# Kernel optimization log

Hardware: AMD Instinct MI355X
Metric: run time of the kernel (lower is better)

Reference implementation:

```python
import jax, jax.numpy as jnp
import numpy as np

L = 50
RHO = 1.0

def _get_index():
    # S = {(m,n) | |mn| <= rho*L//2, |m|<=L/2, |n|<=L/2, n >= |m|}  (index_type 'A')
    S = []
    for m in range(-L // 2, L // 2 + 1):
        for n in range(-L // 2, L // 2 + 1):
            if abs(m * n) <= RHO * L // 2 and n >= abs(m):
                S.append((m, n))
    return np.asarray(S, dtype=np.int32)  # [S, 2], S = 118 for rho=1, L=50


def setup_inputs() -> dict:
    key = jax.random.key(0)
    k1, k2 = jax.random.split(key)
    B, W, M = 2, 16384, 2  # batch, window length, dual-pol modes
    E_real = jax.random.normal(k1, (B, W, M), dtype=jnp.float32)
    E_imag = jax.random.normal(k2, (B, W, M), dtype=jnp.float32)
    return {"E_real": E_real, "E_imag": E_imag}


def _roll_many(E, shifts):
    # torch.roll(E, s, dims=-2) for every s in shifts, vectorized.
    # E: [B, W, M], shifts: [S] -> [B, S, W, M]
    W = E.shape[1]
    idx = (jnp.arange(W)[None, :] - shifts[:, None]) % W  # [S, W]
    return E[:, idx, :]


def _triple(Xa, Xb, Xc):
    # (Xa * conj(Xb) + pol-swap) * Xc  -- the dual-pol (Nmodes=2) term
    A = Xa * jnp.conj(Xb)
    return (A + jnp.roll(A, 1, axis=-1)) * Xc


def _features(E):
    # E: [B, W, M] complex64 -> F: [B, W, M, S] complex64
    idx = _get_index()
    m = jnp.asarray(idx[:, 0])
    n = jnp.asarray(idx[:, 1])
    Rm = _roll_many(E, m)            # roll by m
    Rn = _roll_many(E, n)            # roll by n
    Rmn = _roll_many(E, m + n)       # roll by m+n
    R_m = _roll_many(E, -m)
    R_n = _roll_many(E, -n)
    R_mn = _roll_many(E, -(m + n))
    # Emn + Emn_  (two-term value for generic (m,n))
    T1 = _triple(Rn, Rmn, Rm) + _triple(R_n, R_mn, R_m)
    # Enm + Enm_  (role-swapped terms, added only when n > |m|)
    T2 = _triple(Rm, Rmn, Rn) + _triple(R_m, R_mn, R_n)
    # m=n=0: original computes a single term = T1/2; n>|m|: T1+T2; else (n==|m|, m!=0): T1
    w1 = jnp.where((m == 0) & (n == 0), 0.5, 1.0).astype(jnp.float32)[None, :, None, None]
    w2 = jnp.where(n > jnp.abs(m), 1.0, 0.0).astype(jnp.float32)[None, :, None, None]
    F = w1 * T1 + w2 * T2            # [B, S, W, M]
    return jnp.transpose(F, (0, 2, 3, 1))  # [B, W, M, S]


def reference(E_real, E_imag):
    E = jax.lax.complex(E_real, E_imag)  # complex64
    F = _features(E)
    # split complex output into trailing real/imag channel for a real-valued baseline
    return jnp.stack([jnp.real(F), jnp.imag(F)], axis=-1)  # [B, W, M, S, 2]
```

## Files before the change

kernel.cpp:

```cpp
#include <hip/hip_runtime.h>


constexpr int W = 16384;
constexpr int WMASK = W - 1;
constexpr int NB = 2;
constexpr int S = 118;
constexpr int HALO = 26;
constexpr int TILE_W = 64;
constexpr int LDSW = TILE_W + 2 * HALO;
constexpr int CHUNK = 32;

struct C2 { float re, im; };

__device__ inline void decode_s(int s, int& m, int& n) {
    const int g = (s>=1)+(s>=4)+(s>=10)+(s>=21)+(s>=46)
                + (s>=72)+(s>=97)+(s>=108)+(s>=114)+(s>=117);
    const int start = (s>=117)?117:(s>=114)?114:(s>=108)?108:(s>=97)?97:
                      (s>=72)?72:(s>=46)?46:(s>=21)?21:(s>=10)?10:
                      (s>=4)?4:(s>=1)?1:0;
    m = g - 5;
    const int am = (m < 0) ? -m : m;
    n = am + (s - start);
}

__device__ inline C2 bracket(const float4 a, const float4 b) {
    C2 r;
    r.re = a.x*b.x + a.y*b.y + a.z*b.z + a.w*b.w;
    r.im = a.y*b.x - a.x*b.y + a.w*b.z - a.z*b.w;
    return r;
}

__device__ inline float4 compute_f(const float4 Am, const float4 Ap,
                                   const float4 An, const float4 Bn,
                                   const float4 Amn, const float4 Bmn,
                                   const float w1, const float w2) {
    const C2 B1 = bracket(An, Amn);
    const C2 B2 = bracket(Bn, Bmn);
    float r0 = B1.re*Am.x - B1.im*Am.y + B2.re*Ap.x - B2.im*Ap.y;
    float i0 = B1.re*Am.y + B1.im*Am.x + B2.re*Ap.y + B2.im*Ap.x;
    float r1 = B1.re*Am.z - B1.im*Am.w + B2.re*Ap.z - B2.im*Ap.w;
    float i1 = B1.re*Am.w + B1.im*Am.z + B2.re*Ap.w + B2.im*Ap.z;
    r0 *= w1; i0 *= w1; r1 *= w1; i1 *= w1;
    C2 B3 = bracket(Am, Amn);
    C2 B4 = bracket(Ap, Bmn);
    B3.re *= w2; B3.im *= w2; B4.re *= w2; B4.im *= w2;
    r0 += B3.re*An.x - B3.im*An.y + B4.re*Bn.x - B4.im*Bn.y;
    i0 += B3.re*An.y + B3.im*An.x + B4.re*Bn.y + B4.im*Bn.x;
    r1 += B3.re*An.z - B3.im*An.w + B4.re*Bn.z - B4.im*Bn.w;
    i1 += B3.re*An.w + B3.im*An.z + B4.re*Bn.w + B4.im*Bn.z;
    return make_float4(r0, i0, r1, i1);
}

__global__ __launch_bounds__(256) void sympbc_kernel(
    const float* __restrict__ Er, const float* __restrict__ Ei,
    float* __restrict__ out)
{
    __shared__ float4 eld[LDSW];
    __shared__ float4 obuf[CHUNK][TILE_W];

    const int tid = threadIdx.x;
    const int b = blockIdx.y;
    const int tile0 = blockIdx.x * TILE_W;

    if (tid < LDSW) {
        const int gw = (tile0 - HALO + tid) & WMASK;
        const size_t gi = ((size_t)b * W + gw) * 2;
        const float2 r = *reinterpret_cast<const float2*>(Er + gi);
        const float2 i = *reinterpret_cast<const float2*>(Ei + gi);
        eld[tid] = make_float4(r.x, i.x, r.y, i.y);
    }
    __syncthreads();

    const int lane = tid & 63;
    const int wv   = tid >> 6;
    const int ci   = HALO + lane;

    const int s2    = tid & 31;
    const int wbase = tid >> 5;

    const size_t orow0 = ((size_t)b * W + tile0) * 472;

    #pragma unroll
    for (int chunk = 0; chunk < (S + CHUNK - 1) / CHUNK; ++chunk) {
        const int s_lo = chunk * CHUNK;
        const int s_n  = (S - s_lo < CHUNK) ? (S - s_lo) : CHUNK;

        #pragma unroll
        for (int k = 0; k < CHUNK / 4; ++k) {
            const int sl = wv + 4 * k;
            if (sl < s_n) {
                const int s = s_lo + sl;
                int m, n;
                decode_s(s, m, n);
                const int am = (m < 0) ? -m : m;
                const float w1 = (s == 46) ? 0.5f : 1.0f;
                const float w2 = (n > am) ? 1.0f : 0.0f;

                const float4 Am  = eld[ci - m];
                const float4 Ap  = eld[ci + m];
                const float4 An  = eld[ci - n];
                const float4 Bn  = eld[ci + n];
                const float4 Amn = eld[ci - m - n];
                const float4 Bmn = eld[ci + m + n];

                obuf[sl][lane ^ (sl & 7)] =
                    compute_f(Am, Ap, An, Bn, Amn, Bmn, w1, w2);
            }
        }
        __syncthreads();

        if (s2 < s_n) {
            const size_t scol = (size_t)(s_lo + s2) * 2;
            #pragma unroll
            for (int j = 0; j < TILE_W / 8; ++j) {
                const int w = j * 8 + wbase;
                const float4 F = obuf[s2][w ^ (s2 & 7)];
                float* o = out + orow0 + (size_t)w * 472 + scol;
                *reinterpret_cast<float2*>(o)       = make_float2(F.x, F.y);
                *reinterpret_cast<float2*>(o + 236) = make_float2(F.z, F.w);
            }
        }
        __syncthreads();
    }
}

extern "C" void kernel_launch(void* const* d_in, const int* in_sizes, int n_in,
                              void* d_out, int out_size, void* d_ws, size_t ws_size,
                              hipStream_t stream) {
    const float* Er = (const float*)d_in[0];
    const float* Ei = (const float*)d_in[1];
    float* out = (float*)d_out;
    dim3 grid(W / TILE_W, NB);
    sympbc_kernel<<<grid, dim3(256), 0, stream>>>(Er, Ei, out);
}
```

Before: 24.04 us.

## Split S chunks across grid z dimension and widen output stores to float4

```diff
diff --git a/kernel.cpp b/kernel.cpp
--- a/kernel.cpp
+++ b/kernel.cpp
@@ -8,7 +8,8 @@
 constexpr int HALO = 26;
 constexpr int TILE_W = 64;
 constexpr int LDSW = TILE_W + 2 * HALO;
-constexpr int CHUNK = 32;
+constexpr int CHUNK = 16;
+constexpr int NCHUNK = (S + CHUNK - 1) / CHUNK;
 
 struct C2 { float re, im; };
 
@@ -56,11 +57,13 @@
     float* __restrict__ out)
 {
     __shared__ float4 eld[LDSW];
-    __shared__ float4 obuf[CHUNK][TILE_W];
+    __shared__ float4 obuf[CHUNK][TILE_W + 1];
 
     const int tid = threadIdx.x;
     const int b = blockIdx.y;
     const int tile0 = blockIdx.x * TILE_W;
+    const int s_lo = blockIdx.z * CHUNK;
+    const int s_n = (S - s_lo < CHUNK) ? (S - s_lo) : CHUNK;
 
     if (tid < LDSW) {
         const int gw = (tile0 - HALO + tid) & WMASK;
@@ -74,53 +77,49 @@
     const int lane = tid & 63;
     const int wv   = tid >> 6;
     const int ci   = HALO + lane;
-
-    const int s2    = tid & 31;
-    const int wbase = tid >> 5;
-
-    const size_t orow0 = ((size_t)b * W + tile0) * 472;
+    const float4 Eself = eld[ci];
 
     #pragma unroll
-    for (int chunk = 0; chunk < (S + CHUNK - 1) / CHUNK; ++chunk) {
-        const int s_lo = chunk * CHUNK;
-        const int s_n  = (S - s_lo < CHUNK) ? (S - s_lo) : CHUNK;
+    for (int k = 0; k < CHUNK / 4; ++k) {
+        const int sl = wv + 4 * k;
+        if (sl < s_n) {
+            const int s = s_lo + sl;
+            int m, n;
+            decode_s(s, m, n);
+            const int am = (m < 0) ? -m : m;
+            const float w1 = (s == 46) ? 0.5f : 1.0f;
+            const float w2 = (n > am) ? 1.0f : 0.0f;
+            const int mn = m + n;
 
+            float4 Am, Ap, Amn, Bmn;
+            if (m == 0) { Am = Eself; Ap = Eself; }
+            else        { Am = eld[ci - m]; Ap = eld[ci + m]; }
+            if (mn == 0) { Amn = Eself; Bmn = Eself; }
+            else         { Amn = eld[ci - mn]; Bmn = eld[ci + mn]; }
+            const float4 An = eld[ci - n];
+            const float4 Bn = eld[ci + n];
+
+            obuf[sl][lane] = compute_f(Am, Ap, An, Bn, Amn, Bmn, w1, w2);
+        }
+    }
+    __syncthreads();
+
+    const int sp = tid & 7;
+    const int wq = tid >> 3;
+    if (2 * sp < s_n) {
+        const size_t scol = (size_t)(s_lo + 2 * sp) * 2;
+        const size_t orow0 = ((size_t)b * W + tile0) * 472 + scol;
         #pragma unroll
-        for (int k = 0; k < CHUNK / 4; ++k) {
-            const int sl = wv + 4 * k;
-            if (sl < s_n) {
-                const int s = s_lo + sl;
-                int m, n;
-                decode_s(s, m, n);
-                const int am = (m < 0) ? -m : m;
-                const float w1 = (s == 46) ? 0.5f : 1.0f;
-                const float w2 = (n > am) ? 1.0f : 0.0f;
-
-                const float4 Am  = eld[ci - m];
-                const float4 Ap  = eld[ci + m];
-                const float4 An  = eld[ci - n];
-                const float4 Bn  = eld[ci + n];
-                const float4 Amn = eld[ci - m - n];
-                const float4 Bmn = eld[ci + m + n];
-
-                obuf[sl][lane ^ (sl & 7)] =
-                    compute_f(Am, Ap, An, Bn, Amn, Bmn, w1, w2);
-            }
+        for (int half = 0; half < 2; ++half) {
+            const int w = wq + 32 * half;
+            const float4 F0 = obuf[2 * sp][w];
+            const float4 F1 = obuf[2 * sp + 1][w];
+            float* o = out + orow0 + (size_t)w * 472;
+            *reinterpret_cast<float4*>(o) =
+                make_float4(F0.x, F0.y, F1.x, F1.y);
+            *reinterpret_cast<float4*>(o + 236) =
+                make_float4(F0.z, F0.w, F1.z, F1.w);
         }
-        __syncthreads();
-
-        if (s2 < s_n) {
-            const size_t scol = (size_t)(s_lo + s2) * 2;
-            #pragma unroll
-            for (int j = 0; j < TILE_W / 8; ++j) {
-                const int w = j * 8 + wbase;
-                const float4 F = obuf[s2][w ^ (s2 & 7)];
-                float* o = out + orow0 + (size_t)w * 472 + scol;
-                *reinterpret_cast<float2*>(o)       = make_float2(F.x, F.y);
-                *reinterpret_cast<float2*>(o + 236) = make_float2(F.z, F.w);
-            }
-        }
-        __syncthreads();
     }
 }
 
@@ -130,6 +129,6 @@
     const float* Er = (const float*)d_in[0];
     const float* Ei = (const float*)d_in[1];
     float* out = (float*)d_out;
-    dim3 grid(W / TILE_W, NB);
+    dim3 grid(W / TILE_W, NB, NCHUNK);
     sympbc_kernel<<<grid, dim3(256), 0, stream>>>(Er, Ei, out);
 }
```

New measurement: 24.83 us. 1.03x slower.
